# Optimization experiments

Measured on AMD Instinct MI355X. Metric: run time of the kernel, lower is better.

Reference implementation:

```python
import jax, jax.numpy as jnp
import numpy as np

B, C, H, W = 2, 256, 48, 48
HIDDEN, NUM_HEADS = 512, 8
HEAD_DIM = HIDDEN // NUM_HEADS
EPS = 1e-5


def setup_inputs() -> dict:
    key = jax.random.key(0)
    ks = jax.random.split(key, 16)
    inp = {
        'modal1_feat': jax.random.normal(ks[0], (B, C, H, W), jnp.float32),
        'modal2_feat': jax.random.normal(ks[1], (B, C, H, W), jnp.float32),
    }
    s = 0.02  # weight init scale
    names = ['wq1', 'wk1', 'wv1', 'wq2', 'wk2', 'wv2']
    for i, nm in enumerate(names):
        inp[nm] = jax.random.normal(ks[2 + i], (HIDDEN, C), jnp.float32) * s
        inp['b' + nm[1:]] = jnp.zeros((HIDDEN,), jnp.float32)
    inp['wo1'] = jax.random.normal(ks[8], (C, HIDDEN), jnp.float32) * s
    inp['bo1'] = jnp.zeros((C,), jnp.float32)
    inp['wo2'] = jax.random.normal(ks[9], (C, HIDDEN), jnp.float32) * s
    inp['bo2'] = jnp.zeros((C,), jnp.float32)
    inp['ln1_g'] = jnp.ones((C,), jnp.float32)
    inp['ln1_b'] = jnp.zeros((C,), jnp.float32)
    inp['ln2_g'] = jnp.ones((C,), jnp.float32)
    inp['ln2_b'] = jnp.zeros((C,), jnp.float32)
    inp['wf'] = jax.random.normal(ks[10], (C, 2 * C), jnp.float32) * s
    inp['bf'] = jnp.zeros((C,), jnp.float32)
    inp['bn_g'] = jnp.ones((C,), jnp.float32)
    inp['bn_b'] = jnp.zeros((C,), jnp.float32)
    inp['bn_mean'] = jnp.zeros((C,), jnp.float32)
    inp['bn_var'] = jnp.ones((C,), jnp.float32)
    return inp


def _conv1x1(x, w, b):
    return jnp.einsum('bchw,oc->bohw', x, w) + b[None, :, None, None]


def _ln_channels(x, g, b):
    # LayerNorm over channel dim (x: [B,C,H,W]) applied in NHWC layout
    xc = x.transpose(0, 2, 3, 1)
    mu = xc.mean(-1, keepdims=True)
    var = ((xc - mu) ** 2).mean(-1, keepdims=True)
    y = (xc - mu) / jnp.sqrt(var + EPS) * g + b
    return y.transpose(0, 3, 1, 2)


def reference(modal1_feat, modal2_feat, wq1, bq1, wk1, bk1, wv1, bv1,
              wq2, bq2, wk2, bk2, wv2, bv2, wo1, bo1, wo2, bo2,
              ln1_g, ln1_b, ln2_g, ln2_b, wf, bf, bn_g, bn_b, bn_mean, bn_var):
    b_, c1, h1, w1 = modal1_feat.shape
    hw = h1 * w1
    scale = HEAD_DIM ** -0.5

    def as_q(t):  # [B,hidden,H,W] -> [B,h,L,d]
        return t.reshape(b_, NUM_HEADS, HEAD_DIM, hw).transpose(0, 1, 3, 2)

    def as_k(t):  # [B,h,d,L]
        return t.reshape(b_, NUM_HEADS, HEAD_DIM, hw)

    q1 = as_q(_conv1x1(modal1_feat, wq1, bq1))
    k1 = as_k(_conv1x1(modal1_feat, wk1, bk1))
    v1 = as_q(_conv1x1(modal1_feat, wv1, bv1))
    q2 = as_q(_conv1x1(modal2_feat, wq2, bq2))
    k2 = as_k(_conv1x1(modal2_feat, wk2, bk2))
    v2 = as_q(_conv1x1(modal2_feat, wv2, bv2))

    a12 = jax.nn.softmax(jnp.einsum('bhld,bhdm->bhlm', q1, k2) * scale, axis=-1)
    o1 = jnp.einsum('bhlm,bhmd->bhld', a12, v2).transpose(0, 1, 3, 2).reshape(b_, HIDDEN, h1, w1)
    a21 = jax.nn.softmax(jnp.einsum('bhld,bhdm->bhlm', q2, k1) * scale, axis=-1)
    o2 = jnp.einsum('bhlm,bhmd->bhld', a21, v1).transpose(0, 1, 3, 2).reshape(b_, HIDDEN, h1, w1)

    mod1_cross = _conv1x1(o1, wo1, bo1)
    mod2_cross = _conv1x1(o2, wo2, bo2)

    m1 = _ln_channels(modal1_feat + mod1_cross, ln1_g, ln1_b)
    m2 = _ln_channels(modal2_feat + mod2_cross, ln2_g, ln2_b)

    fused = jnp.concatenate([m1, m2], axis=1)
    f = _conv1x1(fused, wf, bf)
    # BatchNorm2d in eval mode (running stats)
    f = (f - bn_mean[None, :, None, None]) / jnp.sqrt(bn_var + EPS)[None, :, None, None]
    f = f * bn_g[None, :, None, None] + bn_b[None, :, None, None]
    return jax.nn.relu(f)
```

## Files before the change

kernel.cpp:

```cpp
#include <hip/hip_runtime.h>
#include <hip/hip_bf16.h>

#define HW_N 2304
#define EPS_F 1e-5f
#define QSCALE 0.18033688011112043f

typedef float f32x4 __attribute__((ext_vector_type(4)));
typedef float f32x16 __attribute__((ext_vector_type(16)));
typedef unsigned u32x4 __attribute__((ext_vector_type(4)));
typedef short short8v __attribute__((ext_vector_type(8)));
typedef __bf16 bf16x8 __attribute__((ext_vector_type(8)));
typedef unsigned short u16;

__device__ __forceinline__ f32x4 mfma_bf16(bf16x8 a, bf16x8 b, f32x4 c) {
    return __builtin_amdgcn_mfma_f32_16x16x32_bf16(a, b, c, 0, 0, 0);
}
__device__ __forceinline__ f32x16 mfma32(bf16x8 a, bf16x8 b, f32x16 c) {
    return __builtin_amdgcn_mfma_f32_32x32x16_bf16(a, b, c, 0, 0, 0);
}
__device__ __forceinline__ bf16x8 ld8(const void* p) {
    return __builtin_bit_cast(bf16x8, *(const short8v*)p);
}
__device__ __forceinline__ unsigned short bfbits(float v) {
    return __builtin_bit_cast(unsigned short, __float2bfloat16(v));
}
__device__ __forceinline__ float b2f(u16 u) {
    unsigned x = (unsigned)u << 16;
    return __builtin_bit_cast(float, x);
}
__device__ __forceinline__ unsigned pack2(float lo, float hi) {
    return (unsigned)bfbits(lo) | ((unsigned)bfbits(hi) << 16);
}
__device__ __forceinline__ float exp2_fast(float x) {
    float r;
    asm("v_exp_f32 %0, %1" : "=v"(r) : "v"(x));
    return r;
}
__device__ __forceinline__ unsigned cvt_pk(float lo, float hi) {
    unsigned r;
    asm("v_cvt_pk_bf16_f32 %0, %1, %2" : "=v"(r) : "v"(lo), "v"(hi));
    return r;
}
__device__ __forceinline__ f32x16 zero16() {
    f32x16 z;
#pragma unroll
    for (int i = 0; i < 16; ++i) z[i] = 0.f;
    return z;
}

struct WPtrs { const float* s[9]; u16* d[9]; };

__global__ __launch_bounds__(256)
void conv_w_kernel(WPtrs p)
{
    const int j = blockIdx.z;
    const float* s = p.s[j];
    u16* d = p.d[j];
    const int i = (blockIdx.x * 256 + threadIdx.x) * 4;
    const float4 v = *(const float4*)(s + i);
    ushort4 pk;
    pk.x = bfbits(v.x); pk.y = bfbits(v.y); pk.z = bfbits(v.z); pk.w = bfbits(v.w);
    *(ushort4*)(d + i) = pk;
}

__global__ __launch_bounds__(256)
void prep_modal_kernel(const float* __restrict__ m1, const float* __restrict__ m2,
                       u16* __restrict__ t1, u16* __restrict__ t2)
{
    const int l0 = blockIdx.x * 64, c0 = blockIdx.y * 64;
    const int which = blockIdx.z >> 1, b = blockIdx.z & 1;
    const float* src = (which ? m2 : m1) + ((long long)b * 256 + c0) * HW_N + l0;
    u16* dst = (which ? t2 : t1) + ((long long)b * HW_N + l0) * 256 + c0;

    __shared__ float tile[64][65];
    const int t = threadIdx.x;
    const int r = t >> 4, cq = (t & 15) * 4;
#pragma unroll
    for (int i = 0; i < 4; ++i) {
        const int row = r + i * 16;
        const float4 v = *(const float4*)(src + (long long)row * HW_N + cq);
        tile[row][cq + 0] = v.x; tile[row][cq + 1] = v.y;
        tile[row][cq + 2] = v.z; tile[row][cq + 3] = v.w;
    }
    __syncthreads();
#pragma unroll
    for (int i = 0; i < 4; ++i) {
        const int lr = r + i * 16;
        ushort4 pk;
        pk.x = bfbits(tile[cq + 0][lr]);
        pk.y = bfbits(tile[cq + 1][lr]);
        pk.z = bfbits(tile[cq + 2][lr]);
        pk.w = bfbits(tile[cq + 3][lr]);
        *(ushort4*)(dst + (long long)lr * 256 + cq) = pk;
    }
}

struct GArgs {
    const u16* W[6];
    const float* bias[6];
    const u16* X[2];
    const u16* R[2];
    u16* outQ[2]; u16* outK[2]; u16* outV[2];
    float* outT[2];
    float* outC;
    const float *bnm, *bnv, *bng, *bnb;
};

template<int MODE>
__global__ __launch_bounds__(256)
void gemm_mfma(GArgs g)
{
    constexpr int KD = (MODE == 0) ? 256 : 512;
    constexpr int NS = KD / 32;
    const int z = blockIdx.y;
    const int j = blockIdx.z;
    const int mt_b = blockIdx.x / 18;
    const int nt_b = blockIdx.x - mt_b * 18;
    const int m0 = mt_b * 128, n0 = nt_b * 128;

    const u16* Wb = g.W[(MODE == 2) ? 0 : j];
    const u16* Xb0 = (MODE == 0) ? g.X[(j < 3) ? 0 : 1]
                                 : ((MODE == 1) ? g.X[j] : nullptr);

    __shared__ u16 Als[4096];
    __shared__ u16 Bls[4096];

    const int tid = threadIdx.x;
    const int w = tid >> 6, lane = tid & 63;
    const int l16 = lane & 15, lg = lane >> 4;

    const int ar0 = (((tid >> 6) << 4) | (tid & 15));
    const int k8 = (tid >> 4) & 3;

    short8v sa0, sa1, sb0, sb1;

    auto stage = [&](int kb) {
        const int koff = kb + k8 * 8;
        sa0 = *(const short8v*)(Wb + (long long)(m0 + ar0) * KD + koff);
        sa1 = *(const short8v*)(Wb + (long long)(m0 + ar0 + 64) * KD + koff);
        if constexpr (MODE == 0) {
            const u16* p = Xb0 + ((long long)z * HW_N + n0 + ar0) * 256 + koff;
            sb0 = *(const short8v*)p;
            sb1 = *(const short8v*)(p + 64LL * 256);
        } else if constexpr (MODE == 1) {
            const int head = kb >> 6;
            const u16* p = Xb0 + (((long long)z * 8 + head) * HW_N + n0 + ar0) * 64 + (koff & 63);
            sb0 = *(const short8v*)p;
            sb1 = *(const short8v*)(p + 64LL * 64);
        } else {
            const u16* Xb = (kb < 256) ? g.X[0] : g.X[1];
            const u16* p = Xb + ((long long)z * HW_N + n0 + ar0) * 256 + (koff & 255);
            sb0 = *(const short8v*)p;
            sb1 = *(const short8v*)(p + 64LL * 256);
        }
    };

    f32x4 acc[4][4];
#pragma unroll
    for (int a = 0; a < 4; ++a)
#pragma unroll
        for (int b = 0; b < 4; ++b) acc[a][b] = f32x4{0.f, 0.f, 0.f, 0.f};

    stage(0);
    for (int s = 0; s < NS; ++s) {
        __syncthreads();
        *(short8v*)((char*)Als + tid * 16) = sa0;
        *(short8v*)((char*)Als + tid * 16 + 4096) = sa1;
        *(short8v*)((char*)Bls + tid * 16) = sb0;
        *(short8v*)((char*)Bls + tid * 16 + 4096) = sb1;
        __syncthreads();
        if (s + 1 < NS) stage((s + 1) * 32);

        bf16x8 bfr[4];
#pragma unroll
        for (int nt = 0; nt < 4; ++nt)
            bfr[nt] = ld8((char*)Bls + ((w & 1) * 4 + nt) * 1024 + lane * 16);
#pragma unroll
        for (int mt = 0; mt < 4; ++mt) {
            const bf16x8 af = ld8((char*)Als + ((w >> 1) * 4 + mt) * 1024 + lane * 16);
#pragma unroll
            for (int nt = 0; nt < 4; ++nt)
                acc[mt][nt] = mfma_bf16(af, bfr[nt], acc[mt][nt]);
        }
    }

    const int mbase = m0 + (w >> 1) * 64 + 4 * lg;
    const int nbase = n0 + (w & 1) * 64 + l16;

    if constexpr (MODE == 0) {
        const int kind = j % 3, which = j / 3;
        const float* Bp = g.bias[j];
        if (kind < 2) {
            u16* T = (kind == 0) ? g.outQ[which] : g.outK[which];
            const float s = (kind == 0) ? QSCALE : 1.0f;
#pragma unroll
            for (int mt = 0; mt < 4; ++mt) {
                const int m = mbase + mt * 16;
                const float4 bv = *(const float4*)(Bp + m);
#pragma unroll
                for (int nt = 0; nt < 4; ++nt) {
                    const int l = nbase + nt * 16;
                    const f32x4 a = acc[mt][nt];
                    ushort4 pk;
                    pk.x = bfbits((a.x + bv.x) * s);
                    pk.y = bfbits((a.y + bv.y) * s);
                    pk.z = bfbits((a.z + bv.z) * s);
                    pk.w = bfbits((a.w + bv.w) * s);
                    *(ushort4*)(T + ((long long)(z * 8 + (m >> 6)) * HW_N + l) * 64 + (m & 63)) = pk;
                }
            }
        } else {
            u16* V = g.outV[which];
#pragma unroll
            for (int mt = 0; mt < 4; ++mt) {
                const int m = mbase + mt * 16;
                const float4 bv = *(const float4*)(Bp + m);
#pragma unroll
                for (int nt = 0; nt < 4; ++nt) {
                    const int l = nbase + nt * 16;
                    const f32x4 a = acc[mt][nt];
                    V[((long long)z * 512 + m + 0) * HW_N + l] = bfbits(a.x + bv.x);
                    V[((long long)z * 512 + m + 1) * HW_N + l] = bfbits(a.y + bv.y);
                    V[((long long)z * 512 + m + 2) * HW_N + l] = bfbits(a.z + bv.z);
                    V[((long long)z * 512 + m + 3) * HW_N + l] = bfbits(a.w + bv.w);
                }
            }
        }
    } else if constexpr (MODE == 1) {
        const float* Bp = g.bias[j];
        const u16* Rb = g.R[j];
        float* Ob = g.outT[j];
#pragma unroll
        for (int mt = 0; mt < 4; ++mt) {
            const int m = mbase + mt * 16;
            const float4 bv = *(const float4*)(Bp + m);
#pragma unroll
            for (int nt = 0; nt < 4; ++nt) {
                const int l = nbase + nt * 16;
                const long long rowoff = ((long long)z * HW_N + l) * 256 + m;
                const ushort4 rv = *(const ushort4*)(Rb + rowoff);
                const f32x4 a = acc[mt][nt];
                float4 o;
                o.x = a.x + bv.x + b2f(rv.x);
                o.y = a.y + bv.y + b2f(rv.y);
                o.z = a.z + bv.z + b2f(rv.z);
                o.w = a.w + bv.w + b2f(rv.w);
                *(float4*)(Ob + rowoff) = o;
            }
        }
    } else {
        const float* Bp = g.bias[0];
#pragma unroll
        for (int mt = 0; mt < 4; ++mt) {
            const int m = mbase + mt * 16;
            const float4 bv = *(const float4*)(Bp + m);
            const float4 mu = *(const float4*)(g.bnm + m);
            const float4 vr = *(const float4*)(g.bnv + m);
            const float4 ga = *(const float4*)(g.bng + m);
            const float4 be = *(const float4*)(g.bnb + m);
            const float sc0 = ga.x * rsqrtf(vr.x + EPS_F), sh0 = be.x - mu.x * sc0;
            const float sc1 = ga.y * rsqrtf(vr.y + EPS_F), sh1 = be.y - mu.y * sc1;
            const float sc2 = ga.z * rsqrtf(vr.z + EPS_F), sh2 = be.z - mu.z * sc2;
            const float sc3 = ga.w * rsqrtf(vr.w + EPS_F), sh3 = be.w - mu.w * sc3;
#pragma unroll
            for (int nt = 0; nt < 4; ++nt) {
                const int l = nbase + nt * 16;
                const f32x4 a = acc[mt][nt];
                float* O = g.outC + (long long)z * 256 * HW_N + l;
                O[(long long)(m + 0) * HW_N] = fmaxf((a.x + bv.x) * sc0 + sh0, 0.f);
                O[(long long)(m + 1) * HW_N] = fmaxf((a.y + bv.y) * sc1 + sh1, 0.f);
                O[(long long)(m + 2) * HW_N] = fmaxf((a.z + bv.z) * sc2 + sh2, 0.f);
                O[(long long)(m + 3) * HW_N] = fmaxf((a.w + bv.w) * sc3 + sh3, 0.f);
            }
        }
    }
}

__global__ __launch_bounds__(256)
void attn_mfma_kernel(const u16* __restrict__ qt0, const u16* __restrict__ kt0,
                      const u16* __restrict__ v0b,
                      const u16* __restrict__ qt1, const u16* __restrict__ kt1,
                      const u16* __restrict__ v1b,
                      u16* __restrict__ oat0T, u16* __restrict__ oat1T)
{
    const int flat = blockIdx.x;
    const int virt = (flat & 7) * 72 + (flat >> 3);
    const int lt = virt % 18;
    const int hz = virt / 18;
    const int h = hz & 7;
    const int zz = hz >> 3;
    const int b = zz >> 1, dir = zz & 1;

    const u16* QT = dir ? qt1 : qt0;
    const u16* KT = dir ? kt0 : kt1;
    const u16* V  = dir ? v0b : v1b;

    const long long bh = (long long)(b * 8 + h);
    const u16* Qb = QT + bh * HW_N * 64;
    const u16* Kb = KT + bh * HW_N * 64;
    const u16* Vb = V + ((long long)b * 512 + h * 64) * HW_N;

    const int tid = threadIdx.x;
    const int w = tid >> 6, lane = tid & 63;
    const int l32 = lane & 31, hi = lane >> 5;
    const int q0 = lt * 128 + w * 32;

    __shared__ u16 Ks[2][64 * 64];
    __shared__ u16 Vs[2][64 * 64];

    bf16x8 qf0, qf1, qf2, qf3;
    {
        const u16* qrow = Qb + (long long)(q0 + l32) * 64 + 8 * hi;
        qf0 = ld8(qrow);       qf1 = ld8(qrow + 16);
        qf2 = ld8(qrow + 32);  qf3 = ld8(qrow + 48);
    }
    bf16x8 onesv;
    {
        short8v o;
#pragma unroll
        for (int i = 0; i < 8; ++i) o[i] = (short)0x3F80;
        onesv = __builtin_bit_cast(bf16x8, o);
    }

    f32x16 accA = zero16(), accB = zero16(), accs = zero16();
    float m_run = -1e30f;

    auto SWZ = [](int r) { return ((r ^ (r >> 3)) & 7) << 4; };

    const int rsub = lane >> 3;
    const int csub = (lane & 7) * 8;
    const int r0 = 16 * w + rsub, r1 = r0 + 8;
    const int swz0 = (csub * 2) ^ SWZ(r0);
    const int swz1 = (csub * 2) ^ SWZ(r1);

    short8v ka, kb2, va, vb2;
    auto stage = [&](int t) {
        const int m0 = t * 64;
        const u16* kbase = Kb + (long long)(m0 + 16 * w) * 64;
        ka  = *(const short8v*)(kbase + (long long)rsub * 64 + csub);
        kb2 = *(const short8v*)(kbase + (long long)(8 + rsub) * 64 + csub);
        const u16* vbase = Vb + (long long)(16 * w + rsub) * HW_N + m0 + csub;
        va  = *(const short8v*)(vbase);
        vb2 = *(const short8v*)(vbase + 8LL * HW_N);
    };
    auto commit = [&](int buf) {
        *(short8v*)((char*)Ks[buf] + r0 * 128 + swz0) = ka;
        *(short8v*)((char*)Ks[buf] + r1 * 128 + swz1) = kb2;
        *(short8v*)((char*)Vs[buf] + r0 * 128 + swz0) = va;
        *(short8v*)((char*)Vs[buf] + r1 * 128 + swz1) = vb2;
    };

    const int rb0 = l32 * 128;
    const int rb1 = (l32 + 32) * 128;
    const int cs0 = (16 * hi) ^ SWZ(l32);
    const int cs1 = (16 * hi) ^ SWZ(l32 + 32);

    stage(0); commit(0); stage(1);
    __syncthreads();

    for (int t = 0; t < 36; ++t) {
        const int cur = t & 1;
        const char* kbase = (const char*)Ks[cur];
        const char* vbase = (const char*)Vs[cur];

        const bf16x8 kf00 = ld8(kbase + rb0 + (cs0 ^ 0));
        const bf16x8 kf01 = ld8(kbase + rb1 + (cs1 ^ 0));
        const bf16x8 kf10 = ld8(kbase + rb0 + (cs0 ^ 32));
        const bf16x8 kf11 = ld8(kbase + rb1 + (cs1 ^ 32));
        const bf16x8 kf20 = ld8(kbase + rb0 + (cs0 ^ 64));
        const bf16x8 kf21 = ld8(kbase + rb1 + (cs1 ^ 64));
        const bf16x8 kf30 = ld8(kbase + rb0 + (cs0 ^ 96));
        const bf16x8 kf31 = ld8(kbase + rb1 + (cs1 ^ 96));

        if (t + 1 < 36) commit(cur ^ 1);
        if (t + 2 < 36) stage(t + 2);

        f32x16 s0 = zero16(), s1 = zero16();
        __builtin_amdgcn_s_setprio(1);
        s0 = mfma32(kf00, qf0, s0); s1 = mfma32(kf01, qf0, s1);
        s0 = mfma32(kf10, qf1, s0); s1 = mfma32(kf11, qf1, s1);
        s0 = mfma32(kf20, qf2, s0); s1 = mfma32(kf21, qf2, s1);
        s0 = mfma32(kf30, qf3, s0); s1 = mfma32(kf31, qf3, s1);
        __builtin_amdgcn_s_setprio(0);

        const bf16x8 vf00 = ld8(vbase + rb0 + (cs0 ^ 0));
        const bf16x8 vf01 = ld8(vbase + rb1 + (cs1 ^ 0));
        const bf16x8 vf10 = ld8(vbase + rb0 + (cs0 ^ 32));
        const bf16x8 vf11 = ld8(vbase + rb1 + (cs1 ^ 32));
        const bf16x8 vf20 = ld8(vbase + rb0 + (cs0 ^ 64));
        const bf16x8 vf21 = ld8(vbase + rb1 + (cs1 ^ 64));
        const bf16x8 vf30 = ld8(vbase + rb0 + (cs0 ^ 96));
        const bf16x8 vf31 = ld8(vbase + rb1 + (cs1 ^ 96));

        f32x16 mv;
#pragma unroll
        for (int i = 0; i < 16; ++i) mv[i] = fmaxf(s0[i], s1[i]);
        float t0m = fmaxf(fmaxf(mv[0], mv[1]), mv[2]);
        float t1m = fmaxf(fmaxf(mv[3], mv[4]), mv[5]);
        float t2m = fmaxf(fmaxf(mv[6], mv[7]), mv[8]);
        float t3m = fmaxf(fmaxf(mv[9], mv[10]), mv[11]);
        float t4m = fmaxf(fmaxf(mv[12], mv[13]), mv[14]);
        float mx = fmaxf(fmaxf(fmaxf(t0m, t1m), fmaxf(t2m, t3m)), fmaxf(t4m, mv[15]));
        {
            unsigned mu = __builtin_bit_cast(unsigned, mx);
            unsigned mv2 = mu;
            asm("v_permlane32_swap_b32 %0, %1" : "+v"(mu), "+v"(mv2));
            mx = fmaxf(__builtin_bit_cast(float, mu), __builtin_bit_cast(float, mv2));
        }

        if (!__all(mx <= m_run + 8.f)) {
            const float m_new = fmaxf(m_run, mx);
            const float alpha = exp2_fast(m_run - m_new);
#pragma unroll
            for (int i = 0; i < 16; ++i) {
                accA[i] *= alpha; accB[i] *= alpha; accs[i] *= alpha;
            }
            m_run = m_new;
        }

#pragma unroll
        for (int i = 0; i < 16; ++i) {
            s0[i] = exp2_fast(s0[i] - m_run);
            s1[i] = exp2_fast(s1[i] - m_run);
        }

        __builtin_amdgcn_s_setprio(1);
#define PVSTEP(S, PT, VF0, VF1) { \
        constexpr int qe = 2 * ((S) & 1), qo = qe + 1; \
        unsigned a0 = cvt_pk(PT[4 * qe + 0], PT[4 * qe + 1]); \
        unsigned b0 = cvt_pk(PT[4 * qe + 2], PT[4 * qe + 3]); \
        unsigned a1 = cvt_pk(PT[4 * qo + 0], PT[4 * qo + 1]); \
        unsigned b1 = cvt_pk(PT[4 * qo + 2], PT[4 * qo + 3]); \
        asm("v_permlane32_swap_b32 %0, %1" : "+v"(a0), "+v"(a1)); \
        asm("v_permlane32_swap_b32 %0, %1" : "+v"(b0), "+v"(b1)); \
        u32x4 pw = {a0, b0, a1, b1}; \
        const bf16x8 pf = __builtin_bit_cast(bf16x8, pw); \
        accA = mfma32(VF0, pf, accA); \
        accB = mfma32(VF1, pf, accB); \
        accs = mfma32(onesv, pf, accs); }
        PVSTEP(0, s0, vf00, vf01)
        PVSTEP(1, s0, vf10, vf11)
        PVSTEP(2, s1, vf20, vf21)
        PVSTEP(3, s1, vf30, vf31)
#undef PVSTEP
        __builtin_amdgcn_s_setprio(0);

        __syncthreads();
    }

    const float inv = 1.0f / accs[0];
    u16* obase = (dir ? oat1T : oat0T) + (bh * HW_N + q0 + l32) * 64;
#pragma unroll
    for (int g = 0; g < 4; ++g) {
        ushort4 pk;
        pk.x = bfbits(accA[4 * g + 0] * inv);
        pk.y = bfbits(accA[4 * g + 1] * inv);
        pk.z = bfbits(accA[4 * g + 2] * inv);
        pk.w = bfbits(accA[4 * g + 3] * inv);
        *(ushort4*)(obase + 8 * g + 4 * hi) = pk;
        pk.x = bfbits(accB[4 * g + 0] * inv);
        pk.y = bfbits(accB[4 * g + 1] * inv);
        pk.z = bfbits(accB[4 * g + 2] * inv);
        pk.w = bfbits(accB[4 * g + 3] * inv);
        *(ushort4*)(obase + 32 + 8 * g + 4 * hi) = pk;
    }
}

__global__ __launch_bounds__(256)
void ln_t_kernel(const float* __restrict__ mpre0T, const float* __restrict__ mpre1T,
                 const float* __restrict__ g1, const float* __restrict__ b1,
                 const float* __restrict__ g2, const float* __restrict__ b2,
                 u16* __restrict__ mln0T, u16* __restrict__ mln1T)
{
    const int l = blockIdx.x * 64 + (threadIdx.x >> 2);
    const int z = blockIdx.y, dir = blockIdx.z;
    const float* src = (dir ? mpre1T : mpre0T) + ((long long)z * HW_N + l) * 256;
    const float* gg = dir ? g2 : g1;
    const float* bb = dir ? b2 : b1;
    u16* dst = (dir ? mln1T : mln0T) + ((long long)z * HW_N + l) * 256;
    const int q = (threadIdx.x & 3) * 64;

    float4 vbuf[16];
    float sum = 0.f, sq = 0.f;
#pragma unroll
    for (int i = 0; i < 16; ++i) {
        const float4 v = *(const float4*)(src + q + i * 4);
        vbuf[i] = v;
        sum += (v.x + v.y) + (v.z + v.w);
        sq += (v.x * v.x + v.y * v.y) + (v.z * v.z + v.w * v.w);
    }
    sum += __shfl_xor(sum, 1, 64); sum += __shfl_xor(sum, 2, 64);
    sq  += __shfl_xor(sq, 1, 64);  sq  += __shfl_xor(sq, 2, 64);
    const float mean = sum * (1.f / 256.f);
    const float var = sq * (1.f / 256.f) - mean * mean;
    const float rstd = rsqrtf(var + EPS_F);
#pragma unroll
    for (int i = 0; i < 16; ++i) {
        const int c = q + i * 4;
        const float4 gv = *(const float4*)(gg + c);
        const float4 bv = *(const float4*)(bb + c);
        ushort4 pk;
        pk.x = bfbits((vbuf[i].x - mean) * rstd * gv.x + bv.x);
        pk.y = bfbits((vbuf[i].y - mean) * rstd * gv.y + bv.y);
        pk.z = bfbits((vbuf[i].z - mean) * rstd * gv.z + bv.z);
        pk.w = bfbits((vbuf[i].w - mean) * rstd * gv.w + bv.w);
        *(ushort4*)(dst + c) = pk;
    }
}

extern "C" void kernel_launch(void* const* d_in, const int* in_sizes, int n_in,
                              void* d_out, int out_size, void* d_ws, size_t ws_size,
                              hipStream_t stream)
{
    (void)in_sizes; (void)n_in; (void)out_size; (void)ws_size;

    const float* modal1 = (const float*)d_in[0];
    const float* modal2 = (const float*)d_in[1];
    const float* wqkv[6]; const float* bqkv[6];
    for (int j = 0; j < 6; ++j) {
        wqkv[j] = (const float*)d_in[2 + 2 * j];
        bqkv[j] = (const float*)d_in[3 + 2 * j];
    }
    const float* wo1 = (const float*)d_in[14];
    const float* bo1 = (const float*)d_in[15];
    const float* wo2 = (const float*)d_in[16];
    const float* bo2 = (const float*)d_in[17];
    const float* ln1_g = (const float*)d_in[18];
    const float* ln1_b = (const float*)d_in[19];
    const float* ln2_g = (const float*)d_in[20];
    const float* ln2_b = (const float*)d_in[21];
    const float* wf = (const float*)d_in[22];
    const float* bf = (const float*)d_in[23];
    const float* bn_g = (const float*)d_in[24];
    const float* bn_b = (const float*)d_in[25];
    const float* bn_mean = (const float*)d_in[26];
    const float* bn_var = (const float*)d_in[27];

    char* ws = (char*)d_ws;
    size_t off = 0;
    auto alloc = [&](size_t bytes) { char* p = ws + off; off += (bytes + 255) & ~(size_t)255; return p; };

    u16* modalT[2]; u16* wbf[9]; u16* qT[2]; u16* kT[2]; u16* vC[2];
    u16* oatT[2]; float* mpreT[2]; u16* mlnT[2];
    for (int i = 0; i < 2; ++i) modalT[i] = (u16*)alloc(2LL * HW_N * 256 * 2);
    for (int i = 0; i < 9; ++i) wbf[i] = (u16*)alloc(131072 * 2);
    for (int i = 0; i < 2; ++i) qT[i] = (u16*)alloc(2LL * 512 * HW_N * 2);
    for (int i = 0; i < 2; ++i) kT[i] = (u16*)alloc(2LL * 512 * HW_N * 2);
    for (int i = 0; i < 2; ++i) vC[i] = (u16*)alloc(2LL * 512 * HW_N * 2);
    for (int i = 0; i < 2; ++i) oatT[i] = (u16*)alloc(2LL * 512 * HW_N * 2);
    for (int i = 0; i < 2; ++i) mpreT[i] = (float*)alloc(2LL * HW_N * 256 * 4);
    for (int i = 0; i < 2; ++i) mlnT[i] = (u16*)alloc(2LL * HW_N * 256 * 2);

    WPtrs wp;
    for (int j = 0; j < 6; ++j) { wp.s[j] = wqkv[j]; wp.d[j] = wbf[j]; }
    wp.s[6] = wo1; wp.d[6] = wbf[6];
    wp.s[7] = wo2; wp.d[7] = wbf[7];
    wp.s[8] = wf;  wp.d[8] = wbf[8];
    conv_w_kernel<<<dim3(128, 1, 9), 256, 0, stream>>>(wp);
    prep_modal_kernel<<<dim3(36, 4, 4), 256, 0, stream>>>(modal1, modal2, modalT[0], modalT[1]);

    GArgs g0 = {};
    for (int j = 0; j < 6; ++j) { g0.W[j] = wbf[j]; g0.bias[j] = bqkv[j]; }
    g0.X[0] = modalT[0]; g0.X[1] = modalT[1];
    for (int i = 0; i < 2; ++i) { g0.outQ[i] = qT[i]; g0.outK[i] = kT[i]; g0.outV[i] = vC[i]; }
    gemm_mfma<0><<<dim3(72, 2, 6), 256, 0, stream>>>(g0);

    attn_mfma_kernel<<<dim3(576), 256, 0, stream>>>(
        qT[0], kT[0], vC[0], qT[1], kT[1], vC[1], oatT[0], oatT[1]);

    GArgs g1a = {};
    g1a.W[0] = wbf[6]; g1a.W[1] = wbf[7];
    g1a.bias[0] = bo1; g1a.bias[1] = bo2;
    g1a.X[0] = oatT[0]; g1a.X[1] = oatT[1];
    g1a.R[0] = modalT[0]; g1a.R[1] = modalT[1];
    g1a.outT[0] = mpreT[0]; g1a.outT[1] = mpreT[1];
    gemm_mfma<1><<<dim3(36, 2, 2), 256, 0, stream>>>(g1a);

    ln_t_kernel<<<dim3(36, 2, 2), 256, 0, stream>>>(
        mpreT[0], mpreT[1], ln1_g, ln1_b, ln2_g, ln2_b, mlnT[0], mlnT[1]);

    GArgs g2a = {};
    g2a.W[0] = wbf[8]; g2a.bias[0] = bf;
    g2a.X[0] = mlnT[0]; g2a.X[1] = mlnT[1];
    g2a.outC = (float*)d_out;
    g2a.bnm = bn_mean; g2a.bnv = bn_var; g2a.bng = bn_g; g2a.bnb = bn_b;
    gemm_mfma<2><<<dim3(36, 2, 1), 256, 0, stream>>>(g2a);
}
```

Before: 161.4 us.

## Software-pipeline attention loop: overlap next QK^T MFMAs with current softmax/PV

Restructures the flash-attention inner loop into a software pipeline: QK^T scores for tile t+1 are computed while softmax and PV for tile t are done, using two ping-pong score register sets. The LDS ring grows from double to triple buffering so K of the next tile, V of the current tile and the staged commit can coexist. The goal is to hide softmax VALU latency behind MFMA work. It costs extra VGPRs for the second score set and more LDS, which may reduce occupancy.

New measurement: 185.9 us (median of 3 runs). 15.2% more time.

```diff
diff --git a/kernel.cpp b/kernel.cpp
--- a/kernel.cpp
+++ b/kernel.cpp
@@ -27,9 +27,6 @@
 __device__ __forceinline__ float b2f(u16 u) {
     unsigned x = (unsigned)u << 16;
     return __builtin_bit_cast(float, x);
-}
-__device__ __forceinline__ unsigned pack2(float lo, float hi) {
-    return (unsigned)bfbits(lo) | ((unsigned)bfbits(hi) << 16);
 }
 __device__ __forceinline__ float exp2_fast(float x) {
     float r;
@@ -305,8 +302,8 @@
     const int l32 = lane & 31, hi = lane >> 5;
     const int q0 = lt * 128 + w * 32;
 
-    __shared__ u16 Ks[2][64 * 64];
-    __shared__ u16 Vs[2][64 * 64];
+    __shared__ u16 Ks[3][64 * 64];
+    __shared__ u16 Vs[3][64 * 64];
 
     bf16x8 qf0, qf1, qf2, qf3;
     {
@@ -343,11 +340,11 @@
         va  = *(const short8v*)(vbase);
         vb2 = *(const short8v*)(vbase + 8LL * HW_N);
     };
-    auto commit = [&](int buf) {
-        *(short8v*)((char*)Ks[buf] + r0 * 128 + swz0) = ka;
-        *(short8v*)((char*)Ks[buf] + r1 * 128 + swz1) = kb2;
-        *(short8v*)((char*)Vs[buf] + r0 * 128 + swz0) = va;
-        *(short8v*)((char*)Vs[buf] + r1 * 128 + swz1) = vb2;
+    auto commit = [&](char* kd, char* vd) {
+        *(short8v*)(kd + r0 * 128 + swz0) = ka;
+        *(short8v*)(kd + r1 * 128 + swz1) = kb2;
+        *(short8v*)(vd + r0 * 128 + swz0) = va;
+        *(short8v*)(vd + r1 * 128 + swz1) = vb2;
     };
 
     const int rb0 = l32 * 128;
@@ -355,78 +352,59 @@
     const int cs0 = (16 * hi) ^ SWZ(l32);
     const int cs1 = (16 * hi) ^ SWZ(l32 + 32);
 
-    stage(0); commit(0); stage(1);
+    char* k0 = (char*)Ks[0]; char* k1 = (char*)Ks[1]; char* k2 = (char*)Ks[2];
+    char* v0 = (char*)Vs[0]; char* v1 = (char*)Vs[1]; char* v2 = (char*)Vs[2];
+
+    f32x16 sA0, sA1, sB0, sB1;
+
+    stage(0); commit(k0, v0); stage(1);
     __syncthreads();
-
-    for (int t = 0; t < 36; ++t) {
-        const int cur = t & 1;
-        const char* kbase = (const char*)Ks[cur];
-        const char* vbase = (const char*)Vs[cur];
-
-        const bf16x8 kf00 = ld8(kbase + rb0 + (cs0 ^ 0));
-        const bf16x8 kf01 = ld8(kbase + rb1 + (cs1 ^ 0));
-        const bf16x8 kf10 = ld8(kbase + rb0 + (cs0 ^ 32));
-        const bf16x8 kf11 = ld8(kbase + rb1 + (cs1 ^ 32));
-        const bf16x8 kf20 = ld8(kbase + rb0 + (cs0 ^ 64));
-        const bf16x8 kf21 = ld8(kbase + rb1 + (cs1 ^ 64));
-        const bf16x8 kf30 = ld8(kbase + rb0 + (cs0 ^ 96));
-        const bf16x8 kf31 = ld8(kbase + rb1 + (cs1 ^ 96));
-
-        if (t + 1 < 36) commit(cur ^ 1);
-        if (t + 2 < 36) stage(t + 2);
-
-        f32x16 s0 = zero16(), s1 = zero16();
-        __builtin_amdgcn_s_setprio(1);
-        s0 = mfma32(kf00, qf0, s0); s1 = mfma32(kf01, qf0, s1);
-        s0 = mfma32(kf10, qf1, s0); s1 = mfma32(kf11, qf1, s1);
-        s0 = mfma32(kf20, qf2, s0); s1 = mfma32(kf21, qf2, s1);
-        s0 = mfma32(kf30, qf3, s0); s1 = mfma32(kf31, qf3, s1);
-        __builtin_amdgcn_s_setprio(0);
-
-        const bf16x8 vf00 = ld8(vbase + rb0 + (cs0 ^ 0));
-        const bf16x8 vf01 = ld8(vbase + rb1 + (cs1 ^ 0));
-        const bf16x8 vf10 = ld8(vbase + rb0 + (cs0 ^ 32));
-        const bf16x8 vf11 = ld8(vbase + rb1 + (cs1 ^ 32));
-        const bf16x8 vf20 = ld8(vbase + rb0 + (cs0 ^ 64));
-        const bf16x8 vf21 = ld8(vbase + rb1 + (cs1 ^ 64));
-        const bf16x8 vf30 = ld8(vbase + rb0 + (cs0 ^ 96));
-        const bf16x8 vf31 = ld8(vbase + rb1 + (cs1 ^ 96));
-
-        f32x16 mv;
-#pragma unroll
-        for (int i = 0; i < 16; ++i) mv[i] = fmaxf(s0[i], s1[i]);
-        float t0m = fmaxf(fmaxf(mv[0], mv[1]), mv[2]);
-        float t1m = fmaxf(fmaxf(mv[3], mv[4]), mv[5]);
-        float t2m = fmaxf(fmaxf(mv[6], mv[7]), mv[8]);
-        float t3m = fmaxf(fmaxf(mv[9], mv[10]), mv[11]);
-        float t4m = fmaxf(fmaxf(mv[12], mv[13]), mv[14]);
-        float mx = fmaxf(fmaxf(fmaxf(t0m, t1m), fmaxf(t2m, t3m)), fmaxf(t4m, mv[15]));
-        {
-            unsigned mu = __builtin_bit_cast(unsigned, mx);
-            unsigned mv2 = mu;
-            asm("v_permlane32_swap_b32 %0, %1" : "+v"(mu), "+v"(mv2));
-            mx = fmaxf(__builtin_bit_cast(float, mu), __builtin_bit_cast(float, mv2));
-        }
-
-        if (!__all(mx <= m_run + 8.f)) {
-            const float m_new = fmaxf(m_run, mx);
-            const float alpha = exp2_fast(m_run - m_new);
-#pragma unroll
-            for (int i = 0; i < 16; ++i) {
-                accA[i] *= alpha; accB[i] *= alpha; accs[i] *= alpha;
-            }
-            m_run = m_new;
-        }
-
-#pragma unroll
-        for (int i = 0; i < 16; ++i) {
-            s0[i] = exp2_fast(s0[i] - m_run);
-            s1[i] = exp2_fast(s1[i] - m_run);
-        }
-
-        __builtin_amdgcn_s_setprio(1);
-#define PVSTEP(S, PT, VF0, VF1) { \
-        constexpr int qe = 2 * ((S) & 1), qo = qe + 1; \
+    {
+        const bf16x8 kf00 = ld8(k0 + rb0 + (cs0 ^ 0));
+        const bf16x8 kf01 = ld8(k0 + rb1 + (cs1 ^ 0));
+        const bf16x8 kf10 = ld8(k0 + rb0 + (cs0 ^ 32));
+        const bf16x8 kf11 = ld8(k0 + rb1 + (cs1 ^ 32));
+        const bf16x8 kf20 = ld8(k0 + rb0 + (cs0 ^ 64));
+        const bf16x8 kf21 = ld8(k0 + rb1 + (cs1 ^ 64));
+        const bf16x8 kf30 = ld8(k0 + rb0 + (cs0 ^ 96));
+        const bf16x8 kf31 = ld8(k0 + rb1 + (cs1 ^ 96));
+        sA0 = zero16(); sA1 = zero16();
+        sA0 = mfma32(kf00, qf0, sA0); sA1 = mfma32(kf01, qf0, sA1);
+        sA0 = mfma32(kf10, qf1, sA0); sA1 = mfma32(kf11, qf1, sA1);
+        sA0 = mfma32(kf20, qf2, sA0); sA1 = mfma32(kf21, qf2, sA1);
+        sA0 = mfma32(kf30, qf3, sA0); sA1 = mfma32(kf31, qf3, sA1);
+    }
+    commit(k1, v1); stage(2);
+    __syncthreads();
+
+#define SOFTMAX_T(SC0, SC1) { \
+        f32x16 mv_; \
+        _Pragma("unroll") \
+        for (int i = 0; i < 16; ++i) mv_[i] = fmaxf(SC0[i], SC1[i]); \
+        float t0m = fmaxf(fmaxf(mv_[0], mv_[1]), mv_[2]); \
+        float t1m = fmaxf(fmaxf(mv_[3], mv_[4]), mv_[5]); \
+        float t2m = fmaxf(fmaxf(mv_[6], mv_[7]), mv_[8]); \
+        float t3m = fmaxf(fmaxf(mv_[9], mv_[10]), mv_[11]); \
+        float t4m = fmaxf(fmaxf(mv_[12], mv_[13]), mv_[14]); \
+        float mx = fmaxf(fmaxf(fmaxf(t0m, t1m), fmaxf(t2m, t3m)), fmaxf(t4m, mv_[15])); \
+        { unsigned mu = __builtin_bit_cast(unsigned, mx); unsigned mv2 = mu; \
+          asm("v_permlane32_swap_b32 %0, %1" : "+v"(mu), "+v"(mv2)); \
+          mx = fmaxf(__builtin_bit_cast(float, mu), __builtin_bit_cast(float, mv2)); } \
+        if (!__all(mx <= m_run + 8.f)) { \
+            const float m_new = fmaxf(m_run, mx); \
+            const float alpha = exp2_fast(m_run - m_new); \
+            _Pragma("unroll") \
+            for (int i = 0; i < 16; ++i) { accA[i] *= alpha; accB[i] *= alpha; accs[i] *= alpha; } \
+            m_run = m_new; \
+        } \
+        _Pragma("unroll") \
+        for (int i = 0; i < 16; ++i) { \
+            SC0[i] = exp2_fast(SC0[i] - m_run); \
+            SC1[i] = exp2_fast(SC1[i] - m_run); \
+        } }
+
+#define PVSTEP(PT, E, VF0, VF1) { \
+        constexpr int qe = 2 * (E), qo = qe + 1; \
         unsigned a0 = cvt_pk(PT[4 * qe + 0], PT[4 * qe + 1]); \
         unsigned b0 = cvt_pk(PT[4 * qe + 2], PT[4 * qe + 3]); \
         unsigned a1 = cvt_pk(PT[4 * qo + 0], PT[4 * qo + 1]); \
@@ -438,15 +416,68 @@
         accA = mfma32(VF0, pf, accA); \
         accB = mfma32(VF1, pf, accB); \
         accs = mfma32(onesv, pf, accs); }
-        PVSTEP(0, s0, vf00, vf01)
-        PVSTEP(1, s0, vf10, vf11)
-        PVSTEP(2, s1, vf20, vf21)
-        PVSTEP(3, s1, vf30, vf31)
+
+#define ATTN_ITER(t, SC0, SC1, SN0, SN1) { \
+        const bf16x8 kf00 = ld8(k1 + rb0 + (cs0 ^ 0)); \
+        const bf16x8 kf01 = ld8(k1 + rb1 + (cs1 ^ 0)); \
+        const bf16x8 kf10 = ld8(k1 + rb0 + (cs0 ^ 32)); \
+        const bf16x8 kf11 = ld8(k1 + rb1 + (cs1 ^ 32)); \
+        const bf16x8 kf20 = ld8(k1 + rb0 + (cs0 ^ 64)); \
+        const bf16x8 kf21 = ld8(k1 + rb1 + (cs1 ^ 64)); \
+        const bf16x8 kf30 = ld8(k1 + rb0 + (cs0 ^ 96)); \
+        const bf16x8 kf31 = ld8(k1 + rb1 + (cs1 ^ 96)); \
+        const bf16x8 vf00 = ld8(v0 + rb0 + (cs0 ^ 0)); \
+        const bf16x8 vf01 = ld8(v0 + rb1 + (cs1 ^ 0)); \
+        const bf16x8 vf10 = ld8(v0 + rb0 + (cs0 ^ 32)); \
+        const bf16x8 vf11 = ld8(v0 + rb1 + (cs1 ^ 32)); \
+        const bf16x8 vf20 = ld8(v0 + rb0 + (cs0 ^ 64)); \
+        const bf16x8 vf21 = ld8(v0 + rb1 + (cs1 ^ 64)); \
+        const bf16x8 vf30 = ld8(v0 + rb0 + (cs0 ^ 96)); \
+        const bf16x8 vf31 = ld8(v0 + rb1 + (cs1 ^ 96)); \
+        SN0 = zero16(); SN1 = zero16(); \
+        __builtin_amdgcn_s_setprio(1); \
+        SN0 = mfma32(kf00, qf0, SN0); SN1 = mfma32(kf01, qf0, SN1); \
+        SN0 = mfma32(kf10, qf1, SN0); SN1 = mfma32(kf11, qf1, SN1); \
+        SN0 = mfma32(kf20, qf2, SN0); SN1 = mfma32(kf21, qf2, SN1); \
+        SN0 = mfma32(kf30, qf3, SN0); SN1 = mfma32(kf31, qf3, SN1); \
+        __builtin_amdgcn_s_setprio(0); \
+        if ((t) + 2 < 36) commit(k2, v2); \
+        if ((t) + 3 < 36) stage((t) + 3); \
+        SOFTMAX_T(SC0, SC1) \
+        __builtin_amdgcn_s_setprio(1); \
+        PVSTEP(SC0, 0, vf00, vf01) \
+        PVSTEP(SC0, 1, vf10, vf11) \
+        PVSTEP(SC1, 0, vf20, vf21) \
+        PVSTEP(SC1, 1, vf30, vf31) \
+        __builtin_amdgcn_s_setprio(0); \
+        __syncthreads(); \
+        { char* tk = k0; k0 = k1; k1 = k2; k2 = tk; \
+          char* tv = v0; v0 = v1; v1 = v2; v2 = tv; } }
+
+    for (int t = 0; t < 34; t += 2) {
+        ATTN_ITER(t, sA0, sA1, sB0, sB1)
+        ATTN_ITER(t + 1, sB0, sB1, sA0, sA1)
+    }
+    ATTN_ITER(34, sA0, sA1, sB0, sB1)
+
+    {
+        const bf16x8 vf00 = ld8(v0 + rb0 + (cs0 ^ 0));
+        const bf16x8 vf01 = ld8(v0 + rb1 + (cs1 ^ 0));
+        const bf16x8 vf10 = ld8(v0 + rb0 + (cs0 ^ 32));
+        const bf16x8 vf11 = ld8(v0 + rb1 + (cs1 ^ 32));
+        const bf16x8 vf20 = ld8(v0 + rb0 + (cs0 ^ 64));
+        const bf16x8 vf21 = ld8(v0 + rb1 + (cs1 ^ 64));
+        const bf16x8 vf30 = ld8(v0 + rb0 + (cs0 ^ 96));
+        const bf16x8 vf31 = ld8(v0 + rb1 + (cs1 ^ 96));
+        SOFTMAX_T(sB0, sB1)
+        PVSTEP(sB0, 0, vf00, vf01)
+        PVSTEP(sB0, 1, vf10, vf11)
+        PVSTEP(sB1, 0, vf20, vf21)
+        PVSTEP(sB1, 1, vf30, vf31)
+    }
+#undef ATTN_ITER
+#undef SOFTMAX_T
 #undef PVSTEP
-        __builtin_amdgcn_s_setprio(0);
-
-        __syncthreads();
-    }
 
     const float inv = 1.0f / accs[0];
     u16* obase = (dir ? oat1T : oat0T) + (bh * HW_N + q0 + l32) * 64;
```
